# Kernel optimization log

Measured on AMD Instinct MI355X. Metric: run time of the kernel, lower is better.

Reference implementation:

```python
import jax, jax.numpy as jnp
import numpy as np

# edge types from metadata: (src_type, 'to', dst_type)
NODE_SRC = [0, 1, 2, 3, 0, 1, 2, 1, 3, 1]
NODE_DST = [0, 1, 2, 3, 1, 0, 1, 2, 1, 3]
N_NODES = 30000
N_EDGES = 400000
HEADS1 = 8


def _han_conv(xs, edges, proj_W, proj_b, att_src, att_dst, k_W, k_b, q, heads):
    """Faithful port of torch_geometric HANConv (eval mode, dropout off)."""
    out_ch = proj_W.shape[-1]
    D = out_ch // heads
    N = xs[0].shape[0]
    # per-node-type projection -> [N, H, D]
    h = [(xs[t] @ proj_W[t] + proj_b[t]).reshape(N, heads, D) for t in range(4)]
    outs = {t: [] for t in range(4)}
    for e in range(10):
        s, d = NODE_SRC[e], NODE_DST[e]
        row, col = edges[e, 0], edges[e, 1]
        a_src = (h[s] * att_src[e]).sum(-1)  # [N, H]
        a_dst = (h[d] * att_dst[e]).sum(-1)  # [N, H]
        alpha = jax.nn.leaky_relu(a_src[row] + a_dst[col], 0.2)  # [E, H]
        # segment softmax over incoming edges of each dst node
        amax = jax.ops.segment_max(alpha, col, num_segments=N)
        ex = jnp.exp(alpha - amax[col])
        denom = jax.ops.segment_sum(ex, col, num_segments=N)
        w = ex / (denom[col] + 1e-16)
        msg = h[s][row] * w[:, :, None]  # [E, H, D]
        agg = jax.ops.segment_sum(msg, col, num_segments=N).reshape(N, out_ch)
        outs[d].append(jax.nn.relu(agg))
    # semantic-level attention fusion across relations ending at each node type
    res = []
    for t in range(4):
        stk = jnp.stack(outs[t])  # [M, N, C]
        score = (q * jnp.tanh(stk @ k_W + k_b).mean(axis=1)).sum(-1)  # [M]
        sattn = jax.nn.softmax(score)
        res.append((sattn[:, None, None] * stk).sum(0))  # [N, C]
    return res


def setup_inputs() -> dict:
    key = jax.random.key(0)
    ks = jax.random.split(key, 24)
    inp = {}
    for t in range(4):
        inp[f"x{t}"] = jax.random.normal(ks[t], (N_NODES, 256), dtype=jnp.float32)
    inp["edges"] = jax.random.randint(ks[4], (10, 2, N_EDGES), 0, N_NODES, dtype=jnp.int32)
    s = 0.05
    inp["proj1_W"] = jax.random.normal(ks[5], (4, 256, 128), dtype=jnp.float32) * s
    inp["proj1_b"] = jax.random.normal(ks[6], (4, 128), dtype=jnp.float32) * s
    inp["att1_src"] = jax.random.normal(ks[7], (10, 8, 16), dtype=jnp.float32) * s
    inp["att1_dst"] = jax.random.normal(ks[8], (10, 8, 16), dtype=jnp.float32) * s
    inp["k1_W"] = jax.random.normal(ks[9], (128, 128), dtype=jnp.float32) * s
    inp["k1_b"] = jax.random.normal(ks[10], (128,), dtype=jnp.float32) * s
    inp["q1"] = jax.random.normal(ks[11], (128,), dtype=jnp.float32) * s
    inp["proj2_W"] = jax.random.normal(ks[12], (4, 128, 32), dtype=jnp.float32) * s
    inp["proj2_b"] = jax.random.normal(ks[13], (4, 32), dtype=jnp.float32) * s
    inp["att2_src"] = jax.random.normal(ks[14], (10, 1, 32), dtype=jnp.float32) * s
    inp["att2_dst"] = jax.random.normal(ks[15], (10, 1, 32), dtype=jnp.float32) * s
    inp["k2_W"] = jax.random.normal(ks[16], (32, 32), dtype=jnp.float32) * s
    inp["k2_b"] = jax.random.normal(ks[17], (32,), dtype=jnp.float32) * s
    inp["q2"] = jax.random.normal(ks[18], (32,), dtype=jnp.float32) * s
    return inp


def reference(x0, x1, x2, x3, edges,
              proj1_W, proj1_b, att1_src, att1_dst, k1_W, k1_b, q1,
              proj2_W, proj2_b, att2_src, att2_dst, k2_W, k2_b, q2):
    # eval mode: all F.dropout calls are identity
    xs = [x0, x1, x2, x3]
    h = _han_conv(xs, edges, proj1_W, proj1_b, att1_src, att1_dst, k1_W, k1_b, q1, HEADS1)
    h = [jax.nn.elu(v) for v in h]
    o = _han_conv(h, edges, proj2_W, proj2_b, att2_src, att2_dst, k2_W, k2_b, q2, 1)
    # final per-node softmax over channel dim for each node type; stack since all N equal
    return jnp.stack([jax.nn.softmax(v, axis=1) for v in o])  # [4, N, 32]
```

## Files before the change

kernel.cpp:

```cpp
#include <hip/hip_runtime.h>
#include <hip/hip_fp16.h>

#define NN 30000
#define NE 400000
#define NBUCK 59
#define BPR 98
#define EPB 4096
#define CAPREG 12288
#define BCAP 12288

__constant__ int d_SRC[10] = {0,1,2,3,0,1,2,1,3,1};
__constant__ int d_DST[10] = {0,1,2,3,1,0,1,2,1,3};
__constant__ int d_RORD[10] = {1,5,7,9,0,4,2,6,3,8};
__constant__ int d_GORD[10] = {0,4,1,5,7,9,2,6,3,8};
__constant__ int d_FCNT[4] = {2,4,2,2};
__constant__ int d_FREL[4][4] = {{0,5,0,0},{1,4,6,8},{2,7,0,0},{3,9,0,0}};

typedef _Float16 f16x8 __attribute__((ext_vector_type(8)));
typedef float f32x4 __attribute__((ext_vector_type(4)));

struct __attribute__((aligned(8))) h2x2 { __half2 a, b; };

template<int BN, bool AF16>
__global__ __launch_bounds__(256)
void mgemm_k(const float* __restrict__ A, long sA,
             const float* __restrict__ B, long sB,
             const float* __restrict__ bias, long sBias,
             float* __restrict__ C, long sC,
             int M, int K, int N, int relu_a, int epi)
{
    constexpr int BM = 64, BK = 32;
    constexpr int NF = BN / 16;
    constexpr int LDK = BK + 8;
    const int z = blockIdx.z;
    const _Float16* __restrict__ Ah = (const _Float16*)A;
    if constexpr (AF16) Ah += (long)z * sA; else A += (long)z * sA;
    B += (long)z * sB;
    bias += (long)z * sBias;
    C += (long)z * sC;
    const int m0 = blockIdx.x * BM;
    const int n0 = blockIdx.y * BN;
    const int tid = threadIdx.x;
    const int wv = tid >> 6;
    const int l  = tid & 63;
    const int fm = l & 15;
    const int fg = l >> 4;

    __shared__ _Float16 As[BM][LDK];
    __shared__ _Float16 Bs[BN][LDK];
    __shared__ float red[4][BN];

    f32x4 acc[NF];
#pragma unroll
    for (int f = 0; f < NF; ++f) acc[f] = (f32x4){0.f, 0.f, 0.f, 0.f};

    const int arow = tid >> 2;
    const int akc  = (tid & 3) << 3;
    const int grow = m0 + arow;

    for (int k0 = 0; k0 < K; k0 += BK) {
        f16x8 ap;
        if (grow < M) {
            if constexpr (AF16) {
                ap = *(const f16x8*)(Ah + (long)grow * K + k0 + akc);
                if (relu_a) {
#pragma unroll
                    for (int j = 0; j < 8; ++j)
                        ap[j] = ap[j] > (_Float16)0.f ? ap[j] : (_Float16)0.f;
                }
            } else {
                const float* aq = A + (long)grow * K + k0 + akc;
                float4 u0 = *(const float4*)aq;
                float4 u1 = *(const float4*)(aq + 4);
                float v[8] = {u0.x, u0.y, u0.z, u0.w, u1.x, u1.y, u1.z, u1.w};
                if (relu_a) {
#pragma unroll
                    for (int j = 0; j < 8; ++j) v[j] = fmaxf(v[j], 0.f);
                }
#pragma unroll
                for (int j = 0; j < 8; ++j) ap[j] = (_Float16)v[j];
            }
        } else {
#pragma unroll
            for (int j = 0; j < 8; ++j) ap[j] = (_Float16)0.f;
        }
        *(f16x8*)&As[arow][akc] = ap;

        if constexpr (BN == 64) {
            const int bk = tid >> 4;
            const int bn = (tid & 15) << 2;
#pragma unroll
            for (int kk = 0; kk < 2; ++kk) {
                int kr = bk + kk * 16;
                float4 u = *(const float4*)(B + (long)(k0 + kr) * N + n0 + bn);
                Bs[bn + 0][kr] = (_Float16)u.x;
                Bs[bn + 1][kr] = (_Float16)u.y;
                Bs[bn + 2][kr] = (_Float16)u.z;
                Bs[bn + 3][kr] = (_Float16)u.w;
            }
        } else {
            const int bk = tid >> 3;
            const int bn = (tid & 7) << 2;
            float4 u = *(const float4*)(B + (long)(k0 + bk) * N + n0 + bn);
            Bs[bn + 0][bk] = (_Float16)u.x;
            Bs[bn + 1][bk] = (_Float16)u.y;
            Bs[bn + 2][bk] = (_Float16)u.z;
            Bs[bn + 3][bk] = (_Float16)u.w;
        }
        __syncthreads();

        f16x8 a = *(const f16x8*)&As[wv * 16 + fm][fg * 8];
#pragma unroll
        for (int f = 0; f < NF; ++f) {
            f16x8 b = *(const f16x8*)&Bs[f * 16 + fm][fg * 8];
            acc[f] = __builtin_amdgcn_mfma_f32_16x16x32_f16(a, b, acc[f], 0, 0, 0);
        }
        __syncthreads();
    }

    if (epi == 0) {
#pragma unroll
        for (int f = 0; f < NF; ++f) {
            float bz = bias[n0 + f * 16 + fm];
#pragma unroll
            for (int i = 0; i < 4; ++i) {
                int gr = m0 + wv * 16 + fg * 4 + i;
                if (gr < M) C[(long)gr * N + n0 + f * 16 + fm] = acc[f][i] + bz;
            }
        }
    } else if (epi == 2) {
        __half* Ch = (__half*)C;
#pragma unroll
        for (int f = 0; f < NF; ++f) {
            float bz = bias[n0 + f * 16 + fm];
#pragma unroll
            for (int i = 0; i < 4; ++i) {
                int gr = m0 + wv * 16 + fg * 4 + i;
                if (gr < M) Ch[(long)gr * N + n0 + f * 16 + fm] = __float2half(acc[f][i] + bz);
            }
        }
    } else {
#pragma unroll
        for (int f = 0; f < NF; ++f) {
            float bz = bias[n0 + f * 16 + fm];
            float s = 0.f;
#pragma unroll
            for (int i = 0; i < 4; ++i) {
                int gr = m0 + wv * 16 + fg * 4 + i;
                if (gr < M) s += tanhf(acc[f][i] + bz);
            }
            s += __shfl_xor(s, 16, 64);
            s += __shfl_xor(s, 32, 64);
            if (fg == 0) red[wv][f * 16 + fm] = s;
        }
        __syncthreads();
        if (tid < BN) {
            float s = red[0][tid] + red[1][tid] + red[2][tid] + red[3][tid];
            unsafeAtomicAdd(&C[n0 + tid], s);
        }
    }
}

__global__ __launch_bounds__(256)
void init_bincur(int* __restrict__ binCur)
{
    int i = blockIdx.x * 256 + threadIdx.x;
    if (i < 10 * NBUCK) binCur[i] = (i % NBUCK) * CAPREG;
}

__global__ __launch_bounds__(256)
void csr_binA(const int* __restrict__ edges, int* __restrict__ binCur,
              unsigned* __restrict__ binned)
{
    __shared__ int lcnt[NBUCK];
    __shared__ int gbase[NBUCK];
    int rel = blockIdx.x / BPR;
    int blk = blockIdx.x - rel * BPR;
    int base = blk * EPB;
    int tid = threadIdx.x;
    for (int b = tid; b < NBUCK; b += 256) lcnt[b] = 0;
    __syncthreads();
    const int* er = edges + (long)rel * 2 * NE;
    const int* ec = er + NE;
    unsigned pk[16];
    unsigned mt[16];
#pragma unroll
    for (int k = 0; k < 16; ++k) {
        int i = base + k * 256 + tid;
        if (i < NE) {
            int r = er[i];
            int c = ec[i];
            int b = c >> 9;
            int lo = atomicAdd(&lcnt[b], 1);
            pk[k] = ((unsigned)c << 15) | (unsigned)r;
            mt[k] = ((unsigned)b << 16) | (unsigned)lo;
        } else {
            mt[k] = 0xFFFFFFFFu;
        }
    }
    __syncthreads();
    if (tid < NBUCK) gbase[tid] = atomicAdd(&binCur[rel * NBUCK + tid], lcnt[tid]);
    __syncthreads();
    unsigned* bn = binned + (long)rel * NBUCK * CAPREG;
#pragma unroll
    for (int k = 0; k < 16; ++k) {
        if (mt[k] != 0xFFFFFFFFu) {
            int b = mt[k] >> 16;
            int lo = mt[k] & 0xFFFF;
            bn[gbase[b] + lo] = pk[k];
        }
    }
}

__global__ __launch_bounds__(64)
void bucket_scan(const int* __restrict__ binCur, int* __restrict__ bbase,
                 int* __restrict__ off_all)
{
    int rel = blockIdx.x;
    int t = threadIdx.x;
    __shared__ int c[64];
    int v = (t < NBUCK) ? (binCur[rel * NBUCK + t] - t * CAPREG) : 0;
    c[t] = v;
    __syncthreads();
    for (int d = 1; d < 64; d <<= 1) {
        int u = (t >= d) ? c[t - d] : 0;
        __syncthreads();
        c[t] += u;
        __syncthreads();
    }
    if (t < NBUCK) bbase[rel * NBUCK + t] = c[t] - v;
    if (t == 0) off_all[rel * (NN + 1) + NN] = NE;
}

__global__ __launch_bounds__(256)
void csr_binB(const int* __restrict__ binCur, const int* __restrict__ bbase,
              const unsigned* __restrict__ binned,
              int* __restrict__ off_all, int* __restrict__ rows)
{
    __shared__ int cntS[512];
    __shared__ int lcur[512];
    __shared__ int part[256];
    __shared__ int buf[BCAP];
    int rel = blockIdx.x / NBUCK;
    int bkt = blockIdx.x - rel * NBUCK;
    const unsigned* bn = binned + ((long)rel * NBUCK + bkt) * CAPREG;
    int* off = off_all + rel * (NN + 1);
    int* rw = rows + (long)rel * NE;
    int cnt = binCur[rel * NBUCK + bkt] - bkt * CAPREG;
    int gbase = bbase[rel * NBUCK + bkt];
    int nb0 = bkt << 9;
    int nb1 = min(nb0 + 512, NN);
    int nloc = nb1 - nb0;
    int tid = threadIdx.x;

    cntS[tid] = 0; cntS[tid + 256] = 0;
    __syncthreads();
    for (int j = tid; j < cnt; j += 256) {
        int c = (int)(bn[j] >> 15);
        atomicAdd(&cntS[c - nb0], 1);
    }
    __syncthreads();
    int c0 = cntS[2 * tid], c1 = cntS[2 * tid + 1];
    part[tid] = c0 + c1;
    __syncthreads();
    for (int d = 1; d < 256; d <<= 1) {
        int u = (tid >= d) ? part[tid - d] : 0;
        __syncthreads();
        part[tid] += u;
        __syncthreads();
    }
    int pre = (tid == 0) ? 0 : part[tid - 1];
    cntS[2 * tid] = pre;
    cntS[2 * tid + 1] = pre + c0;
    __syncthreads();
    for (int i = tid; i < nloc; i += 256) off[nb0 + i] = gbase + cntS[i];
    lcur[tid] = cntS[tid]; lcur[tid + 256] = cntS[tid + 256];
    __syncthreads();
    if (cnt <= BCAP) {
        for (int j = tid; j < cnt; j += 256) {
            unsigned p = bn[j];
            int r = (int)(p & 0x7FFF);
            int c = (int)(p >> 15);
            int pos = atomicAdd(&lcur[c - nb0], 1);
            buf[pos] = r;
        }
        __syncthreads();
        for (int i = tid; i < cnt; i += 256) rw[gbase + i] = buf[i];
    } else {
        for (int j = tid; j < cnt; j += 256) {
            unsigned p = bn[j];
            int r = (int)(p & 0x7FFF);
            int c = (int)(p >> 15);
            int pos = atomicAdd(&lcur[c - nb0], 1);
            rw[gbase + pos] = r;
        }
    }
}

__global__ __launch_bounds__(256)
void attn_dots1(const __half* __restrict__ h1h,
                const float* __restrict__ att_src,
                const float* __restrict__ att_dst,
                float* __restrict__ asrc, float* __restrict__ adst)
{
    int gid = blockIdx.x * 256 + threadIdx.x;
    int wave = gid >> 6;
    int lane = gid & 63;
    if (wave >= 4 * NN) return;
    int t = wave / NN;
    int n = wave - t * NN;
    __half2 hh = *(const __half2*)&h1h[(long)(t * NN + n) * 128 + 2 * lane];
    float2 hv = __half22float2(hh);
    const int SRCc[10] = {0,1,2,3,0,1,2,1,3,1};
    const int DSTc[10] = {0,1,2,3,1,0,1,2,1,3};
#pragma unroll
    for (int e = 0; e < 10; ++e) {
        if (SRCc[e] == t) {
            float2 av = *(const float2*)&att_src[e * 128 + 2 * lane];
            float p = hv.x * av.x + hv.y * av.y;
#pragma unroll
            for (int off = 1; off < 8; off <<= 1) p += __shfl_xor(p, off, 64);
            if ((lane & 7) == 0) asrc[(long)(e * NN + n) * 8 + (lane >> 3)] = p;
        }
        if (DSTc[e] == t) {
            float2 bv = *(const float2*)&att_dst[e * 128 + 2 * lane];
            float p = hv.x * bv.x + hv.y * bv.y;
#pragma unroll
            for (int off = 1; off < 8; off <<= 1) p += __shfl_xor(p, off, 64);
            if ((lane & 7) == 0) adst[(long)(e * NN + n) * 8 + (lane >> 3)] = p;
        }
    }
}

__global__ __launch_bounds__(256)
void gather_agg1_all(const int* __restrict__ csr_off, const int* __restrict__ csr_rows,
                     const float* __restrict__ asrc1, const float* __restrict__ adst1,
                     const __half* __restrict__ h1h, __half* __restrict__ slots16)
{
    int e = d_GORD[blockIdx.y];
    int node = blockIdx.x * 4 + (threadIdx.x >> 6);
    int lane = threadIdx.x & 63;
    if (node >= NN) return;
    const int* off = csr_off + e * (NN + 1);
    const int* rows = csr_rows + (long)e * NE;
    const float* asrc_e = asrc1 + (long)e * NN * 8;
    const float* adst_e = adst1 + (long)e * NN * 8;
    const _Float16* h1s = (const _Float16*)h1h + (long)d_SRC[e] * NN * 128;
    __half* out = slots16 + (long)e * NN * 128;

    const int g2  = lane >> 4;
    const int s16 = lane & 15;
    const int hv  = s16 >> 1;
    const int eA  = lane >> 3;
    const int hA  = lane & 7;
    int beg = off[node], end = off[node + 1];
    float adA = adst_e[node * 8 + hA];
    float den = (g2 == 0) ? 1e-16f : 0.f;
    float a0 = 0.f, a1 = 0.f, a2 = 0.f, a3 = 0.f;
    float a4 = 0.f, a5 = 0.f, a6 = 0.f, a7 = 0.f;

#define GA1_STEP(i)                                                              \
    {                                                                            \
        int e0 = 4 * (i) + g2;                                                   \
        float wi = __shfl(w, e0 * 8 + hv, 64);                                   \
        int ri = __shfl(r, e0 * 8, 64);                                          \
        f16x8 v = *(const f16x8*)(h1s + (long)ri * 128 + 8 * s16);               \
        den += wi;                                                               \
        a0 += wi * (float)v[0]; a1 += wi * (float)v[1];                          \
        a2 += wi * (float)v[2]; a3 += wi * (float)v[3];                          \
        a4 += wi * (float)v[4]; a5 += wi * (float)v[5];                          \
        a6 += wi * (float)v[6]; a7 += wi * (float)v[7];                          \
    }

    for (int j0 = beg; j0 < end; j0 += 8) {
        int jj = j0 + eA;
        bool ok = jj < end;
        int r = rows[ok ? jj : beg];
        float a = asrc_e[r * 8 + hA] + adA;
        a = a > 0.f ? a : 0.2f * a;
        float w = ok ? __expf(a) : 0.f;
        int cnt = end - j0;
        if (cnt >= 8) {
            GA1_STEP(0) GA1_STEP(1)
        } else if (cnt > 4) {
            GA1_STEP(0) GA1_STEP(1)
        } else {
            GA1_STEP(0)
        }
    }
#undef GA1_STEP
#pragma unroll
    for (int m = 16; m < 64; m <<= 1) {
        a0 += __shfl_xor(a0, m, 64); a1 += __shfl_xor(a1, m, 64);
        a2 += __shfl_xor(a2, m, 64); a3 += __shfl_xor(a3, m, 64);
        a4 += __shfl_xor(a4, m, 64); a5 += __shfl_xor(a5, m, 64);
        a6 += __shfl_xor(a6, m, 64); a7 += __shfl_xor(a7, m, 64);
        den += __shfl_xor(den, m, 64);
    }
    if (g2 == 0) {
        float inv = 1.0f / den;
        f16x8 o;
        o[0] = (_Float16)(a0 * inv); o[1] = (_Float16)(a1 * inv);
        o[2] = (_Float16)(a2 * inv); o[3] = (_Float16)(a3 * inv);
        o[4] = (_Float16)(a4 * inv); o[5] = (_Float16)(a5 * inv);
        o[6] = (_Float16)(a6 * inv); o[7] = (_Float16)(a7 * inv);
        *(f16x8*)((_Float16*)out + (long)node * 128 + 8 * s16) = o;
    }
}

__global__ __launch_bounds__(256)
void fusion_all(const __half* __restrict__ slots16, const float* __restrict__ sattn,
                __half* __restrict__ h1f)
{
    int t = blockIdx.y;
    int idx = blockIdx.x * 256 + threadIdx.x;
    if (idx >= NN * 32) return;
    int c4 = idx & 31;
    int n = idx >> 5;
    long off = (long)n * 128 + c4 * 4;
    int cnt = d_FCNT[t];
    float o0 = 0.f, o1 = 0.f, o2 = 0.f, o3 = 0.f;
    for (int j = 0; j < cnt; ++j) {
        int e = d_FREL[t][j];
        float w = sattn[e];
        const __half* p = slots16 + (long)e * NN * 128 + off;
        float2 v01 = __half22float2(*(const __half2*)p);
        float2 v23 = __half22float2(*(const __half2*)(p + 2));
        o0 += w * fmaxf(v01.x, 0.f);
        o1 += w * fmaxf(v01.y, 0.f);
        o2 += w * fmaxf(v23.x, 0.f);
        o3 += w * fmaxf(v23.y, 0.f);
    }
    o0 = o0 > 0.f ? o0 : __expf(o0) - 1.f;
    o1 = o1 > 0.f ? o1 : __expf(o1) - 1.f;
    o2 = o2 > 0.f ? o2 : __expf(o2) - 1.f;
    o3 = o3 > 0.f ? o3 : __expf(o3) - 1.f;
    __half* q = h1f + (long)t * NN * 128 + off;
    *(__half2*)q = __floats2half2_rn(o0, o1);
    *(__half2*)(q + 2) = __floats2half2_rn(o2, o3);
}

__global__ __launch_bounds__(256)
void attn_dots2(const __half* __restrict__ h2h,
                const float* __restrict__ att_src,
                const float* __restrict__ att_dst,
                float* __restrict__ asrc, float* __restrict__ adst)
{
    int gid = blockIdx.x * 256 + threadIdx.x;
    int p = gid >> 5;
    int l = gid & 31;
    if (p >= 10 * NN) return;
    int e = p / NN, n = p - e * NN;
    int s = d_SRC[e], d = d_DST[e];
    float hs = __half2float(h2h[(long)(s * NN + n) * 32 + l]);
    float hd = __half2float(h2h[(long)(d * NN + n) * 32 + l]);
    float ps = hs * att_src[e * 32 + l];
    float pd = hd * att_dst[e * 32 + l];
#pragma unroll
    for (int off = 1; off < 32; off <<= 1) {
        ps += __shfl_xor(ps, off, 64);
        pd += __shfl_xor(pd, off, 64);
    }
    if (l == 0) { asrc[e * NN + n] = ps; adst[e * NN + n] = pd; }
}

__global__ __launch_bounds__(256)
void gather_agg2(const int* __restrict__ csr_off, const int* __restrict__ csr_rows,
                 const __half* __restrict__ h2h,
                 const float* __restrict__ asrc, const float* __restrict__ adst,
                 __half* __restrict__ agg2h)
{
    int e = d_RORD[blockIdx.y];
    int node = blockIdx.x * 8 + (threadIdx.x >> 5);
    int lane = threadIdx.x & 31;
    if (node >= NN) return;
    const int* off = csr_off + e * (NN + 1);
    const int* rows = csr_rows + (long)e * NE;
    const __half* h2s = h2h + (long)d_SRC[e] * NN * 32;
    const float* as = asrc + e * NN;
    const int slot = lane >> 3;
    const int sub = lane & 7;
    float ad = adst[e * NN + node];
    int beg = off[node], end = off[node + 1];
    float den = (slot == 0) ? 1e-16f : 0.f;
    float a0 = 0.f, a1 = 0.f, a2 = 0.f, a3 = 0.f;

#define GA2_STEP(i)                                                              \
    {                                                                            \
        int e0 = (i) * 4 + slot;                                                 \
        float wi = __shfl(w, e0, 32);                                            \
        int ri = __shfl(r, e0, 32);                                              \
        h2x2 v = *(const h2x2*)(h2s + (long)ri * 32 + 4 * sub);                  \
        float2 f0 = __half22float2(v.a);                                         \
        float2 f1 = __half22float2(v.b);                                         \
        den += wi;                                                               \
        a0 += wi * f0.x; a1 += wi * f0.y; a2 += wi * f1.x; a3 += wi * f1.y;      \
    }

    for (int j0 = beg; j0 < end; j0 += 32) {
        int jj = j0 + lane;
        bool ok = jj < end;
        int r = rows[ok ? jj : beg];
        float a = as[r] + ad;
        a = a > 0.f ? a : 0.2f * a;
        float w = ok ? __expf(a) : 0.f;
        int cnt = end - j0;
        if (cnt >= 32) {
            GA2_STEP(0) GA2_STEP(1) GA2_STEP(2) GA2_STEP(3)
            GA2_STEP(4) GA2_STEP(5) GA2_STEP(6) GA2_STEP(7)
        } else {
            int it = (cnt + 3) >> 2;
            for (int i = 0; i < it; ++i) GA2_STEP(i)
        }
    }
#undef GA2_STEP
#pragma unroll
    for (int m = 8; m < 32; m <<= 1) {
        a0 += __shfl_xor(a0, m, 32);
        a1 += __shfl_xor(a1, m, 32);
        a2 += __shfl_xor(a2, m, 32);
        a3 += __shfl_xor(a3, m, 32);
        den += __shfl_xor(den, m, 32);
    }
    if (slot == 0) {
        float inv = 1.0f / den;
        h2x2 o;
        o.a = __floats2half2_rn(a0 * inv, a1 * inv);
        o.b = __floats2half2_rn(a2 * inv, a3 * inv);
        *(h2x2*)(agg2h + ((long)e * NN + node) * 32 + 4 * sub) = o;
    }
}

__global__ void score_all_k(const float* __restrict__ colsum, const float* __restrict__ q,
                            float* __restrict__ sattn, int C)
{
    __shared__ float sc[10];
    int tid = threadIdx.x;
    if (tid < 10) {
        float s = 0.f;
        for (int c = 0; c < C; ++c) s += q[c] * colsum[tid * C + c];
        sc[tid] = s / (float)NN;
    }
    __syncthreads();
    if (tid < 4) {
        float mx = -1e30f;
        for (int m = 0; m < 10; ++m) if (d_DST[m] == tid) mx = fmaxf(mx, sc[m]);
        float ex[10];
        float sum = 0.f;
        for (int m = 0; m < 10; ++m) {
            ex[m] = 0.f;
            if (d_DST[m] == tid) { ex[m] = __expf(sc[m] - mx); sum += ex[m]; }
        }
        for (int m = 0; m < 10; ++m) if (d_DST[m] == tid) sattn[m] = ex[m] / sum;
    }
}

__global__ __launch_bounds__(256)
void final_softmax(const __half* __restrict__ agg, const float* __restrict__ sattn,
                   float* __restrict__ out)
{
    int gid = blockIdx.x * 256 + threadIdx.x;
    int c = gid & 31;
    int p = gid >> 5;
    if (p >= 4 * NN) return;
    int t = p / NN, n = p - t * NN;
    float f = 0.f;
    for (int m = 0; m < 10; ++m) {
        if (d_DST[m] != t) continue;
        f += sattn[m] * fmaxf(__half2float(agg[(long)(m * NN + n) * 32 + c]), 0.f);
    }
    float mx = f;
#pragma unroll
    for (int off = 1; off < 32; off <<= 1) mx = fmaxf(mx, __shfl_xor(mx, off, 64));
    float ex = __expf(f - mx);
    float sm = ex;
#pragma unroll
    for (int off = 1; off < 32; off <<= 1) sm += __shfl_xor(sm, off, 64);
    out[(long)(t * NN + n) * 32 + c] = ex / sm;
}

extern "C" void kernel_launch(void* const* d_in, const int* in_sizes, int n_in,
                              void* d_out, int out_size, void* d_ws, size_t ws_size,
                              hipStream_t stream) {
    const float* x[4] = {
        (const float*)d_in[0], (const float*)d_in[1],
        (const float*)d_in[2], (const float*)d_in[3]};
    const int* edges = (const int*)d_in[4];
    const float* W1    = (const float*)d_in[5];
    const float* b1    = (const float*)d_in[6];
    const float* att1s = (const float*)d_in[7];
    const float* att1d = (const float*)d_in[8];
    const float* k1W   = (const float*)d_in[9];
    const float* k1b   = (const float*)d_in[10];
    const float* q1    = (const float*)d_in[11];
    const float* W2    = (const float*)d_in[12];
    const float* b2    = (const float*)d_in[13];
    const float* att2s = (const float*)d_in[14];
    const float* att2d = (const float*)d_in[15];
    const float* k2W   = (const float*)d_in[16];
    const float* k2b   = (const float*)d_in[17];
    const float* q2    = (const float*)d_in[18];

    float* W = (float*)d_ws;
    __half* h1h    = (__half*)W;
    __half* h1f    = (__half*)W;
    __half* h2h    = (__half*)(W + 7680000);
    __half* slots16 = (__half*)(W + 15360000);
    __half* agg2h  = (__half*)(W + 15360000);
    unsigned* binned = (unsigned*)(W + 15360000);
    int*   binCur  = (int*)(W + 15360000 + 7249920);
    int*   bbase   = binCur + 640;
    float* asrc1   = W + 34560000;
    float* adst1   = W + 36960000;
    float* asrc2   = W + 36960000;
    float* adst2   = W + 37260000;
    float* colsum1 = W + 39360000;
    float* sattn1  = W + 39361280;
    float* colsum2 = W + 39361296;
    float* sattn2  = W + 39361616;
    int*   csr_off = (int*)(W + 39361640);
    int*   csr_row = csr_off + 300016;

    init_bincur<<<3, 256, 0, stream>>>(binCur);
    csr_binA<<<BPR * 10, 256, 0, stream>>>(edges, binCur, binned);
    bucket_scan<<<10, 64, 0, stream>>>(binCur, bbase, csr_off);
    csr_binB<<<NBUCK * 10, 256, 0, stream>>>(binCur, bbase, binned, csr_off, csr_row);

    hipMemsetAsync(colsum1, 0, 1632L * 4, stream);

    for (int t = 0; t < 4; ++t) {
        mgemm_k<64, false><<<dim3(469, 2, 1), 256, 0, stream>>>(
            x[t], 0, W1 + (long)t * 256 * 128, 0, b1 + t * 128, 0,
            (float*)(h1h + (long)t * NN * 128), 0, NN, 256, 128, 0, 2);
    }

    attn_dots1<<<30000, 256, 0, stream>>>(h1h, att1s, att1d, asrc1, adst1);

    gather_agg1_all<<<dim3(7500, 10), 256, 0, stream>>>(
        csr_off, csr_row, asrc1, adst1, h1h, slots16);

    mgemm_k<64, true><<<dim3(469, 2, 10), 256, 0, stream>>>(
        (const float*)slots16, (long)NN * 128, k1W, 0, k1b, 0,
        colsum1, 128, NN, 128, 128, 1, 1);
    score_all_k<<<1, 64, 0, stream>>>(colsum1, q1, sattn1, 128);

    fusion_all<<<dim3(3750, 4), 256, 0, stream>>>(slots16, sattn1, h1f);

    mgemm_k<32, true><<<dim3(469, 1, 4), 256, 0, stream>>>(
        (const float*)h1f, (long)NN * 128, W2, 128L * 32, b2, 32,
        (float*)h2h, (long)NN * 16, NN, 128, 32, 0, 2);

    attn_dots2<<<37500, 256, 0, stream>>>(h2h, att2s, att2d, asrc2, adst2);
    gather_agg2<<<dim3(3750, 10), 256, 0, stream>>>(
        csr_off, csr_row, h2h, asrc2, adst2, agg2h);

    mgemm_k<32, true><<<dim3(469, 1, 10), 256, 0, stream>>>(
        (const float*)agg2h, (long)NN * 32, k2W, 0, k2b, 0,
        colsum2, 32L, NN, 32, 32, 1, 1);
    score_all_k<<<1, 64, 0, stream>>>(colsum2, q2, sattn2, 32);
    final_softmax<<<15000, 256, 0, stream>>>(agg2h, sattn2, (float*)d_out);
}
```

Baseline: 769.8 us.

## Double GEMM row tile per block and prefetch next edge batch in gather

The MFMA GEMM now computes 128 rows per block instead of 64. Each wave holds two 16-row accumulator fragments that share each B fragment loaded from LDS, and the grid shrinks to match. Separately, the layer-1 gather loop is software-pipelined: the next group's row index and source attention logit are loaded before the current group is accumulated, to hide gather latency. The costs are more accumulator registers and fewer blocks, which may reduce occupancy and load balance.

Result: no change. 761.2 us (-1.1%).

```diff
diff --git a/kernel.cpp b/kernel.cpp
--- a/kernel.cpp
+++ b/kernel.cpp
@@ -29,7 +29,7 @@
              float* __restrict__ C, long sC,
              int M, int K, int N, int relu_a, int epi)
 {
-    constexpr int BM = 64, BK = 32;
+    constexpr int BM = 128, BK = 32, MR = 2;
     constexpr int NF = BN / 16;
     constexpr int LDK = BK + 8;
     const int z = blockIdx.z;
@@ -50,41 +50,51 @@
     __shared__ _Float16 Bs[BN][LDK];
     __shared__ float red[4][BN];
 
-    f32x4 acc[NF];
-#pragma unroll
-    for (int f = 0; f < NF; ++f) acc[f] = (f32x4){0.f, 0.f, 0.f, 0.f};
-
-    const int arow = tid >> 2;
-    const int akc  = (tid & 3) << 3;
+    f32x4 acc[MR][NF];
+#pragma unroll
+    for (int mr = 0; mr < MR; ++mr)
+#pragma unroll
+        for (int f = 0; f < NF; ++f) acc[mr][f] = (f32x4){0.f, 0.f, 0.f, 0.f};
+
+    const int arow = tid >> 1;
+    const int akc  = (tid & 1) << 4;
     const int grow = m0 + arow;
 
     for (int k0 = 0; k0 < K; k0 += BK) {
-        f16x8 ap;
+        f16x8 ap0, ap1;
         if (grow < M) {
             if constexpr (AF16) {
-                ap = *(const f16x8*)(Ah + (long)grow * K + k0 + akc);
+                const _Float16* aq = Ah + (long)grow * K + k0 + akc;
+                ap0 = *(const f16x8*)aq;
+                ap1 = *(const f16x8*)(aq + 8);
                 if (relu_a) {
 #pragma unroll
-                    for (int j = 0; j < 8; ++j)
-                        ap[j] = ap[j] > (_Float16)0.f ? ap[j] : (_Float16)0.f;
+                    for (int j = 0; j < 8; ++j) {
+                        ap0[j] = ap0[j] > (_Float16)0.f ? ap0[j] : (_Float16)0.f;
+                        ap1[j] = ap1[j] > (_Float16)0.f ? ap1[j] : (_Float16)0.f;
+                    }
                 }
             } else {
                 const float* aq = A + (long)grow * K + k0 + akc;
                 float4 u0 = *(const float4*)aq;
                 float4 u1 = *(const float4*)(aq + 4);
-                float v[8] = {u0.x, u0.y, u0.z, u0.w, u1.x, u1.y, u1.z, u1.w};
+                float4 u2 = *(const float4*)(aq + 8);
+                float4 u3 = *(const float4*)(aq + 12);
+                float v[16] = {u0.x,u0.y,u0.z,u0.w, u1.x,u1.y,u1.z,u1.w,
+                               u2.x,u2.y,u2.z,u2.w, u3.x,u3.y,u3.z,u3.w};
                 if (relu_a) {
 #pragma unroll
-                    for (int j = 0; j < 8; ++j) v[j] = fmaxf(v[j], 0.f);
+                    for (int j = 0; j < 16; ++j) v[j] = fmaxf(v[j], 0.f);
                 }
 #pragma unroll
-                for (int j = 0; j < 8; ++j) ap[j] = (_Float16)v[j];
+                for (int j = 0; j < 8; ++j) { ap0[j] = (_Float16)v[j]; ap1[j] = (_Float16)v[j+8]; }
             }
         } else {
 #pragma unroll
-            for (int j = 0; j < 8; ++j) ap[j] = (_Float16)0.f;
-        }
-        *(f16x8*)&As[arow][akc] = ap;
+            for (int j = 0; j < 8; ++j) { ap0[j] = (_Float16)0.f; ap1[j] = (_Float16)0.f; }
+        }
+        *(f16x8*)&As[arow][akc]     = ap0;
+        *(f16x8*)&As[arow][akc + 8] = ap1;
 
         if constexpr (BN == 64) {
             const int bk = tid >> 4;
@@ -109,11 +119,13 @@
         }
         __syncthreads();
 
-        f16x8 a = *(const f16x8*)&As[wv * 16 + fm][fg * 8];
+        f16x8 a0 = *(const f16x8*)&As[wv * 32 + fm][fg * 8];
+        f16x8 a1 = *(const f16x8*)&As[wv * 32 + 16 + fm][fg * 8];
 #pragma unroll
         for (int f = 0; f < NF; ++f) {
             f16x8 b = *(const f16x8*)&Bs[f * 16 + fm][fg * 8];
-            acc[f] = __builtin_amdgcn_mfma_f32_16x16x32_f16(a, b, acc[f], 0, 0, 0);
+            acc[0][f] = __builtin_amdgcn_mfma_f32_16x16x32_f16(a0, b, acc[0][f], 0, 0, 0);
+            acc[1][f] = __builtin_amdgcn_mfma_f32_16x16x32_f16(a1, b, acc[1][f], 0, 0, 0);
         }
         __syncthreads();
     }
@@ -123,10 +135,12 @@
         for (int f = 0; f < NF; ++f) {
             float bz = bias[n0 + f * 16 + fm];
 #pragma unroll
-            for (int i = 0; i < 4; ++i) {
-                int gr = m0 + wv * 16 + fg * 4 + i;
-                if (gr < M) C[(long)gr * N + n0 + f * 16 + fm] = acc[f][i] + bz;
-            }
+            for (int mr = 0; mr < MR; ++mr)
+#pragma unroll
+                for (int i = 0; i < 4; ++i) {
+                    int gr = m0 + wv * 32 + mr * 16 + fg * 4 + i;
+                    if (gr < M) C[(long)gr * N + n0 + f * 16 + fm] = acc[mr][f][i] + bz;
+                }
         }
     } else if (epi == 2) {
         __half* Ch = (__half*)C;
@@ -134,10 +148,12 @@
         for (int f = 0; f < NF; ++f) {
             float bz = bias[n0 + f * 16 + fm];
 #pragma unroll
-            for (int i = 0; i < 4; ++i) {
-                int gr = m0 + wv * 16 + fg * 4 + i;
-                if (gr < M) Ch[(long)gr * N + n0 + f * 16 + fm] = __float2half(acc[f][i] + bz);
-            }
+            for (int mr = 0; mr < MR; ++mr)
+#pragma unroll
+                for (int i = 0; i < 4; ++i) {
+                    int gr = m0 + wv * 32 + mr * 16 + fg * 4 + i;
+                    if (gr < M) Ch[(long)gr * N + n0 + f * 16 + fm] = __float2half(acc[mr][f][i] + bz);
+                }
         }
     } else {
 #pragma unroll
@@ -145,10 +161,12 @@
             float bz = bias[n0 + f * 16 + fm];
             float s = 0.f;
 #pragma unroll
-            for (int i = 0; i < 4; ++i) {
-                int gr = m0 + wv * 16 + fg * 4 + i;
-                if (gr < M) s += tanhf(acc[f][i] + bz);
-            }
+            for (int mr = 0; mr < MR; ++mr)
+#pragma unroll
+                for (int i = 0; i < 4; ++i) {
+                    int gr = m0 + wv * 32 + mr * 16 + fg * 4 + i;
+                    if (gr < M) s += tanhf(acc[mr][f][i] + bz);
+                }
             s += __shfl_xor(s, 16, 64);
             s += __shfl_xor(s, 32, 64);
             if (fg == 0) red[wv][f * 16 + fm] = s;
@@ -372,20 +390,28 @@
         a6 += wi * (float)v[6]; a7 += wi * (float)v[7];                          \
     }
 
-    for (int j0 = beg; j0 < end; j0 += 8) {
+    if (beg < end) {
+        int j0 = beg;
         int jj = j0 + eA;
         bool ok = jj < end;
         int r = rows[ok ? jj : beg];
-        float a = asrc_e[r * 8 + hA] + adA;
-        a = a > 0.f ? a : 0.2f * a;
-        float w = ok ? __expf(a) : 0.f;
-        int cnt = end - j0;
-        if (cnt >= 8) {
-            GA1_STEP(0) GA1_STEP(1)
-        } else if (cnt > 4) {
-            GA1_STEP(0) GA1_STEP(1)
-        } else {
+        float aw = asrc_e[r * 8 + hA] + adA;
+        while (true) {
+            float al = aw > 0.f ? aw : 0.2f * aw;
+            float w = ok ? __expf(al) : 0.f;
+            int j1 = j0 + 8;
+            int rn = r; float awn = 0.f; bool okn = false;
+            if (j1 < end) {
+                int jn = j1 + eA;
+                okn = jn < end;
+                rn = rows[okn ? jn : beg];
+                awn = asrc_e[rn * 8 + hA] + adA;
+            }
+            int cnt = end - j0;
             GA1_STEP(0)
+            if (cnt > 4) { GA1_STEP(1) }
+            if (j1 >= end) break;
+            j0 = j1; r = rn; aw = awn; ok = okn;
         }
     }
 #undef GA1_STEP
@@ -629,7 +655,7 @@
     hipMemsetAsync(colsum1, 0, 1632L * 4, stream);
 
     for (int t = 0; t < 4; ++t) {
-        mgemm_k<64, false><<<dim3(469, 2, 1), 256, 0, stream>>>(
+        mgemm_k<64, false><<<dim3(235, 2, 1), 256, 0, stream>>>(
             x[t], 0, W1 + (long)t * 256 * 128, 0, b1 + t * 128, 0,
             (float*)(h1h + (long)t * NN * 128), 0, NN, 256, 128, 0, 2);
     }
@@ -639,14 +665,14 @@
     gather_agg1_all<<<dim3(7500, 10), 256, 0, stream>>>(
         csr_off, csr_row, asrc1, adst1, h1h, slots16);
 
-    mgemm_k<64, true><<<dim3(469, 2, 10), 256, 0, stream>>>(
+    mgemm_k<64, true><<<dim3(235, 2, 10), 256, 0, stream>>>(
         (const float*)slots16, (long)NN * 128, k1W, 0, k1b, 0,
         colsum1, 128, NN, 128, 128, 1, 1);
     score_all_k<<<1, 64, 0, stream>>>(colsum1, q1, sattn1, 128);
 
     fusion_all<<<dim3(3750, 4), 256, 0, stream>>>(slots16, sattn1, h1f);
 
-    mgemm_k<32, true><<<dim3(469, 1, 4), 256, 0, stream>>>(
+    mgemm_k<32, true><<<dim3(235, 1, 4), 256, 0, stream>>>(
         (const float*)h1f, (long)NN * 128, W2, 128L * 32, b2, 32,
         (float*)h2h, (long)NN * 16, NN, 128, 32, 0, 2);
 
@@ -654,7 +680,7 @@
     gather_agg2<<<dim3(3750, 10), 256, 0, stream>>>(
         csr_off, csr_row, h2h, asrc2, adst2, agg2h);
 
-    mgemm_k<32, true><<<dim3(469, 1, 10), 256, 0, stream>>>(
+    mgemm_k<32, true><<<dim3(235, 1, 10), 256, 0, stream>>>(
         (const float*)agg2h, (long)NN * 32, k2W, 0, k2b, 0,
         colsum2, 32L, NN, 32, 32, 1, 1);
     score_all_k<<<1, 64, 0, stream>>>(colsum2, q2, sattn2, 32);
```
